# Performance work log

Measured on AMD Instinct MI355X. Metric: run time of the kernel, lower is better.

## Reference

```python
import jax, jax.numpy as jnp
import numpy as np

R = 16
ALPHA = 32.0
SCALING = ALPHA / max(1, R)

def setup_inputs() -> dict:
    key = jax.random.key(0)
    ks = jax.random.split(key, 7)
    B_, D, M = 16384, 1024, 4096
    return {
        "x": jax.random.normal(ks[0], (B_, D), dtype=jnp.float32),
        "W0": jax.random.normal(ks[1], (M, D), dtype=jnp.float32) * 0.02,
        "b0": jax.random.normal(ks[2], (M,), dtype=jnp.float32) * 0.02,
        "A": jax.random.normal(ks[3], (R, D), dtype=jnp.float32) * 0.001,
        "B": jax.random.normal(ks[4], (M, R), dtype=jnp.float32) * 0.02,
        "W2": jax.random.normal(ks[5], (1, M), dtype=jnp.float32) * 0.02,
        "b2": jax.random.normal(ks[6], (1,), dtype=jnp.float32) * 0.02,
    }

def reference(x, W0, b0, A, B, W2, b2):
    # effective_W = W0 + scaling * (B @ A)  -> [m_hidden, d_in]
    W_eff = W0 + SCALING * (B @ A)
    # F.linear(x, W_eff, b0): x @ W_eff^T + b0 -> [batch, m_hidden]
    h = jax.nn.relu(jnp.einsum('bd,md->bm', x, W_eff) + b0)
    # fc2: [batch, 1] then squeeze(-1)
    out = (jnp.einsum('bm,om->bo', h, W2) + b2).squeeze(-1)
    return out
```

## Files before the change

kernel.cpp:

```cpp
#include <hip/hip_runtime.h>
#include <hip/hip_bf16.h>
#include <stdint.h>

#define BATCH  16384
#define D_IN   1024
#define M_HID  4096
#define R_LORA 16
#define SCALING 2.0f


#define STRIP    64
#define NTHREADS 512

typedef __bf16 bf16x8 __attribute__((ext_vector_type(8)));
typedef float  f32x16 __attribute__((ext_vector_type(16)));

__device__ __forceinline__ unsigned f2bf(float f) {
    union { float f; unsigned u; } c; c.f = f;
    unsigned u = c.u;
    return ((u + 0x7FFFu + ((u >> 16) & 1u)) >> 16);
}

__global__ __launch_bounds__(256) void k_wprep(
    const float* __restrict__ W0, const float* __restrict__ A,
    const float* __restrict__ Bl, unsigned short* __restrict__ wb)
{
    __shared__ float A4[8192];
    __shared__ float Bs[512];
    __shared__ unsigned short floc[16384];

    const int tid   = threadIdx.x;
    const int n32   = blockIdx.x >> 1;
    const int chalf = blockIdx.x & 1;
    const int col0  = chalf * 512;

    {
        const float4* Asrc = (const float4*)A;
#pragma unroll
        for (int i = 0; i < 8; ++i) {
            int idx = i * 256 + tid;
            int r = idx >> 7, h = (idx >> 6) & 1, ll = idx & 63;
            ((float4*)A4)[idx] = Asrc[r * 256 + (col0 >> 2) + ll * 2 + h];
        }
        Bs[tid]       = SCALING * Bl[n32 * 512 + tid];
        Bs[tid + 256] = SCALING * Bl[n32 * 512 + 256 + tid];
    }
    __syncthreads();

    const int w = tid >> 6;
    const int l = tid & 63;

    float acc[8][8];
#pragma unroll
    for (int jj = 0; jj < 8; ++jj) {
        const int row = w * 8 + jj;
        const float* p = W0 + (size_t)(n32 * 32 + row) * D_IN + col0 + l * 8;
        float4 v0 = *(const float4*)(p);
        float4 v1 = *(const float4*)(p + 4);
        acc[jj][0] = v0.x; acc[jj][1] = v0.y; acc[jj][2] = v0.z; acc[jj][3] = v0.w;
        acc[jj][4] = v1.x; acc[jj][5] = v1.y; acc[jj][6] = v1.z; acc[jj][7] = v1.w;
    }
#pragma unroll
    for (int r = 0; r < R_LORA; ++r) {
        float4 a0 = ((const float4*)A4)[r * 128 + l];
        float4 a1 = ((const float4*)A4)[r * 128 + 64 + l];
        const float av[8] = { a0.x, a0.y, a0.z, a0.w, a1.x, a1.y, a1.z, a1.w };
#pragma unroll
        for (int jj = 0; jj < 8; ++jj) {
            float s = Bs[(w * 8 + jj) * 16 + r];
#pragma unroll
            for (int k = 0; k < 8; ++k) acc[jj][k] += s * av[k];
        }
    }

#pragma unroll
    for (int jj = 0; jj < 8; ++jj) {
        const int row = w * 8 + jj;
        uint4 o;
        o.x = f2bf(acc[jj][0]) | (f2bf(acc[jj][1]) << 16);
        o.y = f2bf(acc[jj][2]) | (f2bf(acc[jj][3]) << 16);
        o.z = f2bf(acc[jj][4]) | (f2bf(acc[jj][5]) << 16);
        o.w = f2bf(acc[jj][6]) | (f2bf(acc[jj][7]) << 16);
        *(uint4*)((char*)floc + l * 512 + ((row ^ (l & 7)) << 4)) = o;
    }
    __syncthreads();

    unsigned short* gdst = wb + (size_t)n32 * 32768 + chalf * 16384;
#pragma unroll
    for (int i = 0; i < 8; ++i) {
        int L16 = i * 256 + tid;
        int ll = L16 >> 5, rr = L16 & 31;
        uint4 v = *(const uint4*)((const char*)floc + ll * 512 + ((rr ^ (ll & 7)) << 4));
        *(uint4*)(gdst + (size_t)L16 * 8) = v;
    }
}

__global__ __launch_bounds__(NTHREADS, 2) void k_strip(
    const float* __restrict__ xf, const unsigned short* __restrict__ wb,
    const float* __restrict__ b0, const float* __restrict__ W2,
    const float* __restrict__ b2, float* __restrict__ out)
{
    __shared__ unsigned short As[STRIP * D_IN];
    __shared__ float red[8][STRIP];

    const int tid  = threadIdx.x;
    const int lane = tid & 63;
    const int wave = tid >> 6;
    const int rl   = lane & 31;
    const int half = lane >> 5;
    const int row0 = blockIdx.x * STRIP;

    {
        const int r  = tid >> 3;
        const int c0 = tid & 7;
        const float* xr = xf + (size_t)(row0 + r) * D_IN;
#pragma unroll
        for (int i = 0; i < 16; ++i) {
            int c = i * 8 + c0;
            float4 v0 = *(const float4*)(xr + c * 8);
            float4 v1 = *(const float4*)(xr + c * 8 + 4);
            uint4 o;
            o.x = f2bf(v0.x) | (f2bf(v0.y) << 16);
            o.y = f2bf(v0.z) | (f2bf(v0.w) << 16);
            o.z = f2bf(v1.x) | (f2bf(v1.y) << 16);
            o.w = f2bf(v1.z) | (f2bf(v1.w) << 16);
            *(uint4*)(&As[c * 512 + r * 8]) = o;
        }
    }
    __syncthreads();

    float rowpart[2][16];
#pragma unroll
    for (int ti = 0; ti < 2; ++ti)
#pragma unroll
        for (int r = 0; r < 16; ++r) rowpart[ti][r] = 0.f;

    for (int pass = 0; pass < 8; ++pass) {
        const int n0 = wave * 64 + pass * 512;
        const float w2a = W2[n0 + rl],      b0a = b0[n0 + rl];
        const float w2b = W2[n0 + 32 + rl], b0b = b0[n0 + 32 + rl];
        const int n32 = wave * 2 + pass * 16;
        const unsigned short* w0p = wb + (size_t)n32 * 32768 + half * 256 + rl * 8;
        const unsigned short* w1p = w0p + 32768;

        f32x16 acc[2][2] = {};
        bf16x8 wf0[4], wf1[4];
#pragma unroll
        for (int p = 0; p < 4; ++p) {
            wf0[p] = *(const bf16x8*)(w0p + p * 512);
            wf1[p] = *(const bf16x8*)(w1p + p * 512);
        }

#pragma unroll 4
        for (int kk = 0; kk < 64; ++kk) {
            const int cur = kk & 3;
            const int coff = (kk * 2 + half) * 512 + rl * 8;
            bf16x8 af0 = *(const bf16x8*)(&As[coff]);
            bf16x8 af1 = *(const bf16x8*)(&As[coff + 256]);
            bf16x8 w0c = wf0[cur], w1c = wf1[cur];
            if (kk < 60) {
                wf0[cur] = *(const bf16x8*)(w0p + (kk + 4) * 512);
                wf1[cur] = *(const bf16x8*)(w1p + (kk + 4) * 512);
            }
            acc[0][0] = __builtin_amdgcn_mfma_f32_32x32x16_bf16(af0, w0c, acc[0][0], 0, 0, 0);
            acc[0][1] = __builtin_amdgcn_mfma_f32_32x32x16_bf16(af0, w1c, acc[0][1], 0, 0, 0);
            acc[1][0] = __builtin_amdgcn_mfma_f32_32x32x16_bf16(af1, w0c, acc[1][0], 0, 0, 0);
            acc[1][1] = __builtin_amdgcn_mfma_f32_32x32x16_bf16(af1, w1c, acc[1][1], 0, 0, 0);
        }

#pragma unroll
        for (int ti = 0; ti < 2; ++ti)
#pragma unroll
            for (int r = 0; r < 16; ++r)
                rowpart[ti][r] += fmaxf(acc[ti][0][r] + b0a, 0.f) * w2a
                                + fmaxf(acc[ti][1][r] + b0b, 0.f) * w2b;
    }

#pragma unroll
    for (int ti = 0; ti < 2; ++ti)
#pragma unroll
        for (int r = 0; r < 16; ++r) {
            float p = rowpart[ti][r];
#pragma unroll
            for (int m = 1; m <= 16; m <<= 1)
                p += __shfl_xor(p, m, 64);
            if (rl == 0)
                red[wave][ti * 32 + (r & 3) + 8 * (r >> 2) + 4 * half] = p;
        }
    __syncthreads();
    if (tid < STRIP) {
        float s = b2[0];
#pragma unroll
        for (int w = 0; w < 8; ++w) s += red[w][tid];
        out[row0 + tid] = s;
    }
}

__global__ __launch_bounds__(256) void k_naive(
    const float* __restrict__ x, const float* __restrict__ W0,
    const float* __restrict__ b0, const float* __restrict__ A,
    const float* __restrict__ Bl, const float* __restrict__ W2,
    const float* __restrict__ b2, float* __restrict__ out)
{
    __shared__ float xs[D_IN];
    int b = blockIdx.x;
    for (int d = threadIdx.x; d < D_IN; d += 256) xs[d] = x[(size_t)b * D_IN + d];
    __syncthreads();
    float part = 0.f;
    for (int m = threadIdx.x; m < M_HID; m += 256) {
        float h = b0[m];
        const float* wr = W0 + (size_t)m * D_IN;
        const float* brow = Bl + m * R_LORA;
        for (int d = 0; d < D_IN; ++d) {
            float w = wr[d];
            for (int r = 0; r < R_LORA; ++r) w += SCALING * brow[r] * A[r * D_IN + d];
            h += xs[d] * w;
        }
        part += fmaxf(h, 0.f) * W2[m];
    }
    __shared__ float sred[256];
    sred[threadIdx.x] = part;
    __syncthreads();
    for (int s = 128; s > 0; s >>= 1) {
        if (threadIdx.x < s) sred[threadIdx.x] += sred[threadIdx.x + s];
        __syncthreads();
    }
    if (threadIdx.x == 0) out[b] = sred[0] + b2[0];
}

extern "C" void kernel_launch(void* const* d_in, const int* in_sizes, int n_in,
                              void* d_out, int out_size, void* d_ws, size_t ws_size,
                              hipStream_t stream) {
    const float* x  = (const float*)d_in[0];
    const float* W0 = (const float*)d_in[1];
    const float* b0 = (const float*)d_in[2];
    const float* A  = (const float*)d_in[3];
    const float* Bl = (const float*)d_in[4];
    const float* W2 = (const float*)d_in[5];
    const float* b2 = (const float*)d_in[6];
    float* out = (float*)d_out;

    const size_t wb_bytes = (size_t)M_HID * D_IN * 2;
    if (ws_size >= wb_bytes) {
        unsigned short* wb = (unsigned short*)d_ws;
        hipLaunchKernelGGL(k_wprep, dim3(256), dim3(256), 0, stream,
                           W0, A, Bl, wb);
        hipLaunchKernelGGL(k_strip, dim3(BATCH / STRIP), dim3(NTHREADS), 0, stream,
                           x, wb, b0, W2, b2, out);
    } else {
        hipLaunchKernelGGL(k_naive, dim3(BATCH), dim3(256), 0, stream,
                           x, W0, b0, A, Bl, W2, b2, out);
    }
}
```

Before: 248.2 us.

## Add 2D-tiled bf16 MFMA GEMM with pre-converted x and atomic fc2 reduction

Adds a new path that first converts x to bf16 in pre-swizzled 256x64 tiles and writes the merged LoRA weight in a matching transposed tiled layout. A 2D-tiled 256x256 MFMA GEMM then double-buffers the tiles through LDS, applies bias, ReLU and the W2 dot product in registers, and atomically adds partial row sums into an output pre-filled with b2. This replaces the row-strip kernel that streamed the whole weight matrix for every batch strip, so each weight and x tile is reused across a full 256x256 output block. The cost is an extra pass to convert x to bf16, extra workspace, and float atomics whose ordering makes the result nondeterministic.

```diff
diff --git a/kernel.cpp b/kernel.cpp
--- a/kernel.cpp
+++ b/kernel.cpp
@@ -21,9 +21,38 @@
     return ((u + 0x7FFFu + ((u >> 16) & 1u)) >> 16);
 }
 
-__global__ __launch_bounds__(256) void k_wprep(
+
+__global__ __launch_bounds__(256) void k_xprep(
+    const float* __restrict__ xf, const float* __restrict__ b2,
+    unsigned short* __restrict__ xb, float* __restrict__ out)
+{
+    const int tid  = threadIdx.x;
+    const int tile = blockIdx.x;
+    const int mt   = tile >> 4, kt = tile & 15;
+    if (tile < 64) out[tile * 256 + tid] = b2[0];
+
+    unsigned short* dst = xb + (size_t)tile * 16384;
+    const float* src0 = xf + (size_t)(mt * 256) * D_IN + kt * 64;
+#pragma unroll
+    for (int i = 0; i < 8; ++i) {
+        int u  = i * 256 + tid;
+        int r  = u >> 3;
+        int c8 = (u & 7) ^ (r & 7);
+        const float* p = src0 + (size_t)r * D_IN + c8 * 8;
+        float4 v0 = *(const float4*)(p);
+        float4 v1 = *(const float4*)(p + 4);
+        uint4 o;
+        o.x = f2bf(v0.x) | (f2bf(v0.y) << 16);
+        o.y = f2bf(v0.z) | (f2bf(v0.w) << 16);
+        o.z = f2bf(v1.x) | (f2bf(v1.y) << 16);
+        o.w = f2bf(v1.z) | (f2bf(v1.w) << 16);
+        *(uint4*)(dst + (size_t)u * 8) = o;
+    }
+}
+
+__global__ __launch_bounds__(256) void k_wprepT(
     const float* __restrict__ W0, const float* __restrict__ A,
-    const float* __restrict__ Bl, unsigned short* __restrict__ wb)
+    const float* __restrict__ Bl, unsigned short* __restrict__ wbT)
 {
     __shared__ float A4[8192];
     __shared__ float Bs[512];
@@ -73,6 +102,183 @@
         }
     }
 
+#pragma unroll
+    for (int jj = 0; jj < 8; ++jj) {
+        const int row = w * 8 + jj;
+        uint4 o;
+        o.x = f2bf(acc[jj][0]) | (f2bf(acc[jj][1]) << 16);
+        o.y = f2bf(acc[jj][2]) | (f2bf(acc[jj][3]) << 16);
+        o.z = f2bf(acc[jj][4]) | (f2bf(acc[jj][5]) << 16);
+        o.w = f2bf(acc[jj][6]) | (f2bf(acc[jj][7]) << 16);
+        *(uint4*)((char*)floc + l * 512 + ((row ^ (l & 7)) << 4)) = o;
+    }
+    __syncthreads();
+
+    const int nt   = n32 >> 3;
+    const int base = (n32 & 7) * 32;
+#pragma unroll
+    for (int ktl = 0; ktl < 8; ++ktl) {
+        const int kt = chalf * 8 + ktl;
+        const int rl = tid >> 3;
+        const int c8 = (tid & 7) ^ (rl & 7);
+        uint4 v = *(const uint4*)((const char*)floc
+                  + (ktl * 8 + c8) * 512 + ((rl ^ c8) << 4));
+        *(uint4*)(wbT + ((size_t)(nt * 16 + kt) * 2048 + base * 8 + tid) * 8) = v;
+    }
+}
+
+__global__ __launch_bounds__(512, 2) void k_gemm(
+    const unsigned short* __restrict__ xb, const unsigned short* __restrict__ wbT,
+    const float* __restrict__ b0, const float* __restrict__ W2,
+    float* __restrict__ out)
+{
+    __shared__ unsigned short Abuf[2][16384];
+    __shared__ unsigned short Bbuf[2][16384];
+    __shared__ float red[8][128];
+
+    const int tid  = threadIdx.x;
+    const int lane = tid & 63, wave = tid >> 6;
+    const int rl   = lane & 31, half = lane >> 5;
+    const int wm   = wave >> 2, wn = wave & 3;
+    const int rx   = rl & 7;
+
+    const int swz = (blockIdx.x & 7) * 128 + (blockIdx.x >> 3);
+    const int nt  = swz >> 6, mt = swz & 63;
+
+    const unsigned short* asrc = xb  + (size_t)(mt * 16) * 16384;
+    const unsigned short* bsrc = wbT + (size_t)(nt * 16) * 16384;
+
+    uint4 ra[4], rb[4];
+#define GLOAD(KT)                                                            \
+    {                                                                        \
+        const uint4* ap = (const uint4*)(asrc + (size_t)(KT) * 16384);       \
+        const uint4* bp = (const uint4*)(bsrc + (size_t)(KT) * 16384);       \
+        _Pragma("unroll")                                                    \
+        for (int i_ = 0; i_ < 4; ++i_) {                                     \
+            ra[i_] = ap[i_ * 512 + tid];                                     \
+            rb[i_] = bp[i_ * 512 + tid];                                     \
+        }                                                                    \
+    }
+#define DSWRITE(BUF)                                                         \
+    {                                                                        \
+        _Pragma("unroll")                                                    \
+        for (int i_ = 0; i_ < 4; ++i_) {                                     \
+            *(uint4*)((char*)Abuf[BUF] + (i_ * 512 + tid) * 16) = ra[i_];    \
+            *(uint4*)((char*)Bbuf[BUF] + (i_ * 512 + tid) * 16) = rb[i_];    \
+        }                                                                    \
+    }
+
+    GLOAD(0); DSWRITE(0); __syncthreads();
+    GLOAD(1);
+
+    f32x16 acc[4][2] = {};
+
+    for (int kt = 0; kt < 16; ++kt) {
+        const char* Ap = (const char*)Abuf[kt & 1] + (wm * 128 + rl) * 128;
+        const char* Bp = (const char*)Bbuf[kt & 1] + (wn * 64 + rl) * 128;
+#pragma unroll
+        for (int s = 0; s < 4; ++s) {
+            const int off = ((2 * s + half) ^ rx) << 4;
+            bf16x8 a0  = *(const bf16x8*)(Ap + off);
+            bf16x8 a1  = *(const bf16x8*)(Ap + 4096  + off);
+            bf16x8 a2  = *(const bf16x8*)(Ap + 8192  + off);
+            bf16x8 a3  = *(const bf16x8*)(Ap + 12288 + off);
+            bf16x8 bv0 = *(const bf16x8*)(Bp + off);
+            bf16x8 bv1 = *(const bf16x8*)(Bp + 4096  + off);
+            acc[0][0] = __builtin_amdgcn_mfma_f32_32x32x16_bf16(a0, bv0, acc[0][0], 0, 0, 0);
+            acc[0][1] = __builtin_amdgcn_mfma_f32_32x32x16_bf16(a0, bv1, acc[0][1], 0, 0, 0);
+            acc[1][0] = __builtin_amdgcn_mfma_f32_32x32x16_bf16(a1, bv0, acc[1][0], 0, 0, 0);
+            acc[1][1] = __builtin_amdgcn_mfma_f32_32x32x16_bf16(a1, bv1, acc[1][1], 0, 0, 0);
+            acc[2][0] = __builtin_amdgcn_mfma_f32_32x32x16_bf16(a2, bv0, acc[2][0], 0, 0, 0);
+            acc[2][1] = __builtin_amdgcn_mfma_f32_32x32x16_bf16(a2, bv1, acc[2][1], 0, 0, 0);
+            acc[3][0] = __builtin_amdgcn_mfma_f32_32x32x16_bf16(a3, bv0, acc[3][0], 0, 0, 0);
+            acc[3][1] = __builtin_amdgcn_mfma_f32_32x32x16_bf16(a3, bv1, acc[3][1], 0, 0, 0);
+        }
+        if (kt < 15) {
+            DSWRITE((kt & 1) ^ 1);
+            __syncthreads();
+            if (kt < 14) GLOAD(kt + 2);
+        }
+    }
+
+    const int n0 = nt * 256 + wn * 64;
+    const float w2a = W2[n0 + rl],      b0a = b0[n0 + rl];
+    const float w2b = W2[n0 + 32 + rl], b0b = b0[n0 + 32 + rl];
+#pragma unroll
+    for (int ti = 0; ti < 4; ++ti)
+#pragma unroll
+        for (int r = 0; r < 16; ++r) {
+            float p = fmaxf(acc[ti][0][r] + b0a, 0.f) * w2a
+                    + fmaxf(acc[ti][1][r] + b0b, 0.f) * w2b;
+#pragma unroll
+            for (int m = 1; m <= 16; m <<= 1)
+                p += __shfl_xor(p, m, 64);
+            if (rl == 0)
+                red[wave][ti * 32 + (r & 3) + 8 * (r >> 2) + 4 * half] = p;
+        }
+    __syncthreads();
+    if (tid < 256) {
+        const int wmf = tid >> 7, q = tid & 127;
+        float s = red[wmf * 4 + 0][q] + red[wmf * 4 + 1][q]
+                + red[wmf * 4 + 2][q] + red[wmf * 4 + 3][q];
+        atomicAdd(&out[(size_t)mt * 256 + tid], s);
+    }
+#undef GLOAD
+#undef DSWRITE
+}
+
+
+__global__ __launch_bounds__(256) void k_wprep(
+    const float* __restrict__ W0, const float* __restrict__ A,
+    const float* __restrict__ Bl, unsigned short* __restrict__ wb)
+{
+    __shared__ float A4[8192];
+    __shared__ float Bs[512];
+    __shared__ unsigned short floc[16384];
+
+    const int tid   = threadIdx.x;
+    const int n32   = blockIdx.x >> 1;
+    const int chalf = blockIdx.x & 1;
+    const int col0  = chalf * 512;
+
+    {
+        const float4* Asrc = (const float4*)A;
+#pragma unroll
+        for (int i = 0; i < 8; ++i) {
+            int idx = i * 256 + tid;
+            int r = idx >> 7, h = (idx >> 6) & 1, ll = idx & 63;
+            ((float4*)A4)[idx] = Asrc[r * 256 + (col0 >> 2) + ll * 2 + h];
+        }
+        Bs[tid]       = SCALING * Bl[n32 * 512 + tid];
+        Bs[tid + 256] = SCALING * Bl[n32 * 512 + 256 + tid];
+    }
+    __syncthreads();
+
+    const int w = tid >> 6;
+    const int l = tid & 63;
+
+    float acc[8][8];
+#pragma unroll
+    for (int jj = 0; jj < 8; ++jj) {
+        const int row = w * 8 + jj;
+        const float* p = W0 + (size_t)(n32 * 32 + row) * D_IN + col0 + l * 8;
+        float4 v0 = *(const float4*)(p);
+        float4 v1 = *(const float4*)(p + 4);
+        acc[jj][0] = v0.x; acc[jj][1] = v0.y; acc[jj][2] = v0.z; acc[jj][3] = v0.w;
+        acc[jj][4] = v1.x; acc[jj][5] = v1.y; acc[jj][6] = v1.z; acc[jj][7] = v1.w;
+    }
+#pragma unroll
+    for (int r = 0; r < R_LORA; ++r) {
+        float4 a0 = ((const float4*)A4)[r * 128 + l];
+        float4 a1 = ((const float4*)A4)[r * 128 + 64 + l];
+        const float av[8] = { a0.x, a0.y, a0.z, a0.w, a1.x, a1.y, a1.z, a1.w };
+#pragma unroll
+        for (int jj = 0; jj < 8; ++jj) {
+            float s = Bs[(w * 8 + jj) * 16 + r];
+#pragma unroll
+            for (int k = 0; k < 8; ++k) acc[jj][k] += s * av[k];
+        }
+    }
 #pragma unroll
     for (int jj = 0; jj < 8; ++jj) {
         const int row = w * 8 + jj;
@@ -241,9 +447,20 @@
     float* out = (float*)d_out;
 
     const size_t wb_bytes = (size_t)M_HID * D_IN * 2;
-    if (ws_size >= wb_bytes) {
+    const size_t xb_bytes = (size_t)BATCH * D_IN * 2;
+
+    if (ws_size >= wb_bytes + xb_bytes) {
+        unsigned short* wbT = (unsigned short*)d_ws;
+        unsigned short* xb  = (unsigned short*)((char*)d_ws + wb_bytes);
+        hipLaunchKernelGGL(k_xprep, dim3(1024), dim3(256), 0, stream,
+                           x, b2, xb, out);
+        hipLaunchKernelGGL(k_wprepT, dim3(M_HID / 32 * 2), dim3(256), 0, stream,
+                           W0, A, Bl, wbT);
+        hipLaunchKernelGGL(k_gemm, dim3(1024), dim3(512), 0, stream,
+                           xb, wbT, b0, W2, out);
+    } else if (ws_size >= wb_bytes) {
         unsigned short* wb = (unsigned short*)d_ws;
-        hipLaunchKernelGGL(k_wprep, dim3(256), dim3(256), 0, stream,
+        hipLaunchKernelGGL(k_wprep, dim3(M_HID / 32 * 2), dim3(256), 0, stream,
                            W0, A, Bl, wb);
         hipLaunchKernelGGL(k_strip, dim3(BATCH / STRIP), dim3(NTHREADS), 0, stream,
                            x, wb, b0, W2, b2, out);
```

Measured after the change: 468.3 us. 1.89x slower.
